# Optimization experiments

Measured on AMD Instinct MI355X. Metric: run time of the kernel, lower is better.

The kernel has to match this reference:

```python
import jax, jax.numpy as jnp
import numpy as np

LINHAS, COLUNAS, DIM, BATCH = 64, 64, 512, 256
N_NEURONS = LINHAS * COLUNAS
TAXA_INICIAL = 0.5
SIGMA_INICIAL = max(LINHAS, COLUNAS) / 2.0  # 32.0


def _grid_locations():
    # Matches tf.meshgrid (default 'xy' indexing) -> stack -> reshape(-1, 2)
    x = jnp.arange(LINHAS, dtype=jnp.float32)
    y = jnp.arange(COLUNAS, dtype=jnp.float32)
    gx, gy = jnp.meshgrid(x, y)  # 'xy' indexing, shapes (COLUNAS, LINHAS)
    return jnp.stack([gx, gy], axis=-1).reshape(-1, 2)  # (N_NEURONS, 2)


def setup_inputs() -> dict:
    key = jax.random.key(0)
    kx, kw = jax.random.split(key)
    X = jax.random.normal(kx, (BATCH, DIM), dtype=jnp.float32)
    # keras 'random_normal' initializer: stddev 0.05
    pesos = jax.random.normal(kw, (N_NEURONS, DIM), dtype=jnp.float32) * 0.05
    return {
        "X": X,
        "pesos": pesos,
        "localizacoes": _grid_locations(),
        "passo_atual": 10,
        "total_passos": 1000,
    }


def reference(X, pesos, localizacoes, passo_atual, total_passos):
    decay = jnp.exp(jnp.float32(-passo_atual / total_passos))
    taxa = TAXA_INICIAL * decay
    sigma = SIGMA_INICIAL * decay

    # Euclidean cdist^2: (B, N)
    x2 = jnp.sum(X * X, axis=1, keepdims=True)            # (B, 1)
    w2 = jnp.sum(pesos * pesos, axis=1)                   # (N,)
    dist = x2 + w2 - 2.0 * (X @ pesos.T)                  # (B, N)

    bmu_idx = jnp.argmin(dist, axis=1)                    # (B,)
    bmu_loc = localizacoes[bmu_idx]                       # (B, 2)

    # Squared grid distance from every neuron to each sample's BMU: (B, N)
    diff = localizacoes[None, :, :] - bmu_loc[:, None, :]
    dist_grade = jnp.sum(diff * diff, axis=2)
    h = jnp.exp(-dist_grade / (2.0 * sigma * sigma))      # (B, N)

    # delta_total[n, d] = taxa * mean_b h[b, n] * (X[b, d] - pesos[n, d])
    # computed without materializing the (B, N, D) delta tensor.
    B = jnp.float32(X.shape[0])
    hX = jnp.einsum("bn,bd->nd", h, X)                    # (N, D)
    h_sum = jnp.sum(h, axis=0)                            # (N,)
    delta_total = (taxa / B) * (hX - h_sum[:, None] * pesos)

    new_pesos = pesos + delta_total
    return new_pesos, taxa, sigma
```

## Files before the change

### kernel.cpp

```cpp
#include <hip/hip_runtime.h>
#include <hip/hip_bf16.h>

typedef unsigned int u32;
typedef unsigned short u16;
typedef unsigned long long u64;

#define BATCH 256
#define NN 4096
#define DIM 512

using short8 = __attribute__((ext_vector_type(8))) short;
using f32x4  = __attribute__((ext_vector_type(4))) float;

__device__ inline float b2f(u16 u){ u32 i = ((u32)u)<<16; float f; __builtin_memcpy(&f,&i,4); return f; }
__device__ inline u16 f2b(float v){ __hip_bfloat16 h = __float2bfloat16(v); u16 r; __builtin_memcpy(&r,&h,2); return r; }

__device__ inline float ldv(const void* p, size_t i, int isbf){
  return isbf ? b2f(((const u16*)p)[i]) : ((const float*)p)[i];
}
__device__ inline void stv(void* p, size_t i, float v, int isbf){
  if (isbf) ((__hip_bfloat16*)p)[i] = __float2bfloat16(v);
  else ((float*)p)[i] = v;
}

__device__ inline int sniff(const void* X, int t, int* sh){
  if (t < 64){
    u32 v = ((const u32*)X)[t];
    u16 lo = (u16)(v & 0xffffu);
    int e = (lo >> 7) & 0xff;
    int sane = ((lo & 0x7fffu) == 0) || (e >= 110 && e <= 132);
    u64 m = __ballot(sane);
    if (t == 0) *sh = (__popcll(m) >= 32) ? 1 : 0;
  }
  __syncthreads();
  return *sh;
}

__global__ __launch_bounds__(256) void k_prep(const void* X, const void* W,
    u64* pack, float* w2, u16* XT, u16* Xb, u16* Wb,
    const int* passo, const int* total, void* out){
  __shared__ int sflag;
  int t = threadIdx.x;
  int isbf = sniff(X, t, &sflag);
  int blk = blockIdx.x;
  if (blk < 512){
    int d = blk;
    float v = ldv(X, (size_t)t*DIM + d, isbf);
    XT[(size_t)d*BATCH + t] = f2b(v);
    if (!isbf){
      size_t i = (size_t)d*256 + t;
      Xb[i] = f2b(((const float*)X)[i]);
    }
  } else {
    int j = blk - 512;
    int n0 = j*8;
    int wv = t>>6, lane = t&63;
    #pragma unroll
    for (int rr=0; rr<2; ++rr){
      int n = n0 + wv*2 + rr;
      float xv[8]; float s = 0.f;
      if (isbf){
        short8 x = *(const short8*)((const u16*)W + (size_t)n*DIM + lane*8);
        #pragma unroll
        for (int q=0;q<8;q++) xv[q] = b2f((u16)x[q]);
      } else {
        #pragma unroll
        for (int q=0;q<8;q++) xv[q] = ((const float*)W)[(size_t)n*DIM + lane*8 + q];
      }
      #pragma unroll
      for (int q=0;q<8;q++) s += xv[q]*xv[q];
      #pragma unroll
      for (int off=32; off; off>>=1) s += __shfl_down(s, off);
      if (lane == 0) w2[n] = s;
      if (!isbf){
        #pragma unroll
        for (int q=0;q<8;q++) Wb[(size_t)n*DIM + lane*8 + q] = f2b(xv[q]);
      }
    }
    if (j == 0){
      pack[t] = ~0ull;
      if (t == 0){
        float decay = expf(-(float)passo[0]/(float)total[0]);
        stv(out, (size_t)NN*DIM,     0.5f*decay, isbf);
        stv(out, (size_t)NN*DIM + 1, 32.f*decay, isbf);
      }
    }
  }
}

__global__ __launch_bounds__(256) void k_score(const void* X, const void* W,
    const u16* Xws, const u16* Wws, const float* w2, u64* pack){
  __shared__ int sflag;
  __shared__ float sval[4][32];
  __shared__ int   sidx[4][32];
  int t = threadIdx.x;
  int isbf = sniff(X, t, &sflag);
  const u16* Xb = isbf ? (const u16*)X : Xws;
  const u16* Wb = isbf ? (const u16*)W : Wws;
  int wv = t>>6, l = t&63;
  int lr = l&15, lg = l>>4;

  int id = blockIdx.x;
  int xcd = id & 7, sub = id >> 3;
  int ny = xcd*4 + (sub>>3);
  int bx = sub & 7;
  int b0 = bx*32;
  int n0 = ny*128 + wv*32;

  const u16* xp0 = Xb + (size_t)(b0 + lr)*DIM + lg*8;
  const u16* xp1 = xp0 + (size_t)16*DIM;
  const u16* wp0 = Wb + (size_t)(n0 + lr)*DIM + lg*8;
  const u16* wp1 = wp0 + (size_t)16*DIM;

  f32x4 acc00 = {0,0,0,0}, acc01 = {0,0,0,0}, acc10 = {0,0,0,0}, acc11 = {0,0,0,0};
  #pragma unroll
  for (int ks=0; ks<16; ++ks){
    short8 a0 = *(const short8*)(xp0 + ks*32);
    short8 a1 = *(const short8*)(xp1 + ks*32);
    short8 w0 = *(const short8*)(wp0 + ks*32);
    short8 w1 = *(const short8*)(wp1 + ks*32);
    acc00 = __builtin_amdgcn_mfma_f32_16x16x32_bf16(a0, w0, acc00, 0,0,0);
    acc01 = __builtin_amdgcn_mfma_f32_16x16x32_bf16(a0, w1, acc01, 0,0,0);
    acc10 = __builtin_amdgcn_mfma_f32_16x16x32_bf16(a1, w0, acc10, 0,0,0);
    acc11 = __builtin_amdgcn_mfma_f32_16x16x32_bf16(a1, w1, acc11, 0,0,0);
  }

  float w20 = w2[n0 + lr];
  float w21 = w2[n0 + 16 + lr];
  #pragma unroll
  for (int bb=0; bb<2; ++bb){
    #pragma unroll
    for (int r=0;r<4;++r){
      float s0 = w20 - 2.f*(bb ? acc10[r] : acc00[r]);
      float s1 = w21 - 2.f*(bb ? acc11[r] : acc01[r]);
      float bv; int bi;
      if (s0 <= s1){ bv = s0; bi = n0 + lr; } else { bv = s1; bi = n0 + 16 + lr; }
      #pragma unroll
      for (int m=1; m<16; m<<=1){
        float ov = __shfl_xor(bv, m);
        int   oi = __shfl_xor(bi, m);
        if (ov < bv || (ov == bv && oi < bi)){ bv = ov; bi = oi; }
      }
      if (lr == 0){ int bl = bb*16 + lg*4 + r; sval[wv][bl] = bv; sidx[wv][bl] = bi; }
    }
  }
  __syncthreads();
  if (t < 32){
    float bv = sval[0][t]; int bi = sidx[0][t];
    #pragma unroll
    for (int w4=1; w4<4; ++w4){
      float ov = sval[w4][t]; int oi = sidx[w4][t];
      if (ov < bv || (ov == bv && oi < bi)){ bv = ov; bi = oi; }
    }
    u32 sb = __float_as_uint(bv);
    sb = (sb & 0x80000000u) ? ~sb : (sb | 0x80000000u);
    atomicMin(pack + b0 + t, ((u64)sb << 32) | (u32)bi);
  }
}

__global__ __launch_bounds__(512) void k_update(const void* X, const u16* XT, const void* W,
    const u64* pack, const int* passo, const int* total, void* out){
  __shared__ int sflag;
  __shared__ u16 hT[16][264];
  __shared__ float hpart[8][8];
  __shared__ float hs[16];
  int t = threadIdx.x;
  int isbf = sniff(X, t, &sflag);
  int wv = t>>6, l = t&63;
  int n0 = blockIdx.x * 16;

  float decay = expf(-(float)passo[0] / (float)total[0]);
  float taxa = 0.5f*decay, sigma = 32.f*decay;
  float inv2s2 = 1.f/(2.f*sigma*sigma);

  {
    int b = t & 255;
    int rbase = (t >> 8) * 8;
    int m = (int)(u32)(pack[b] & 0xffffffffu);
    int mx = m & 63, my = m >> 6;
    float hv[8];
    #pragma unroll
    for (int i=0;i<8;++i){
      int n = n0 + rbase + i;
      int dx = (n & 63) - mx;
      int dy = (n >> 6) - my;
      float h = expf(-(float)(dx*dx + dy*dy) * inv2s2);
      hv[i] = h;
      hT[rbase + i][b] = f2b(h);
    }
    #pragma unroll
    for (int i=0;i<8;++i){
      float s = hv[i];
      #pragma unroll
      for (int off=32; off; off>>=1) s += __shfl_down(s, off);
      if (l == 0) hpart[wv][i] = s;
    }
  }
  __syncthreads();
  if (t < 16){
    int g = (t >> 3) * 4;
    hs[t] = hpart[g][t&7] + hpart[g+1][t&7] + hpart[g+2][t&7] + hpart[g+3][t&7];
  }
  __syncthreads();

  int lr = l & 15, lg = l >> 4;
  int d0 = wv * 64;
  f32x4 acc[4];
  #pragma unroll
  for (int f=0;f<4;++f) acc[f] = (f32x4){0.f,0.f,0.f,0.f};

  #pragma unroll
  for (int ks=0; ks<8; ++ks){
    short8 a = *(const short8*)(&hT[lr][ks*32 + lg*8]);
    #pragma unroll
    for (int f=0; f<4; ++f){
      short8 bfr = *(const short8*)(XT + (size_t)(d0 + f*16 + lr)*BATCH + ks*32 + lg*8);
      acc[f] = __builtin_amdgcn_mfma_f32_16x16x32_bf16(a, bfr, acc[f], 0,0,0);
    }
  }

  float cc = taxa / (float)BATCH;
  #pragma unroll
  for (int r=0;r<4;++r){
    int n = n0 + lg*4 + r;
    float hsv = hs[lg*4 + r];
    #pragma unroll
    for (int f=0;f<4;++f){
      size_t gi = (size_t)n*DIM + d0 + f*16 + lr;
      float wv_ = ldv(W, gi, isbf);
      float o = wv_ + cc*(acc[f][r] - hsv*wv_);
      stv(out, gi, o, isbf);
    }
  }
}

extern "C" void kernel_launch(void* const* d_in, const int* in_sizes, int n_in,
                              void* d_out, int out_size, void* d_ws, size_t ws_size,
                              hipStream_t stream) {
  const void* X = d_in[0];
  const void* W = d_in[1];
  const int* passo = (const int*)d_in[3];
  const int* total = (const int*)d_in[4];

  char* ws = (char*)d_ws;
  u64* pack = (u64*)(ws + 256);
  float* w2 = (float*)(ws + 2304);
  u16* XT   = (u16*)(ws + 18688);
  u16* Xb   = (u16*)(ws + 280832);
  u16* Wb   = (u16*)(ws + 542976);

  k_prep  <<<1024, 256, 0, stream>>>(X, W, pack, w2, XT, Xb, Wb, passo, total, d_out);
  k_score <<<256, 256, 0, stream>>>(X, W, Xb, Wb, w2, pack);
  k_update<<<NN/16, 512, 0, stream>>>(X, XT, W, pack, passo, total, d_out);
}
```

Before: 38.84 us.

## Fuse prep, score and update into one cooperative kernel with grid syncs

Merges the three kernel launches into a single cooperative kernel of 256 blocks of 512 threads, separating the phases with grid-wide barriers. Work per block in each phase is remapped so the scoring GEMM uses 8 waves with two MFMA tiles each instead of 4 waves with four. The aim is to remove launch gaps and inter-kernel drain between phases. In exchange it pays for two grid syncs and caps the grid at 256 blocks, and it falls back to the old three-kernel path if the cooperative launch fails.

```diff
diff --git a/kernel.cpp b/kernel.cpp
--- a/kernel.cpp
+++ b/kernel.cpp
@@ -1,5 +1,8 @@
 #include <hip/hip_runtime.h>
 #include <hip/hip_bf16.h>
+#include <hip/hip_cooperative_groups.h>
+
+namespace cg = cooperative_groups;
 
 typedef unsigned int u32;
 typedef unsigned short u16;
@@ -34,6 +37,185 @@
   }
   __syncthreads();
   return *sh;
+}
+
+__global__ __launch_bounds__(512) void k_fused(const void* X, const void* W,
+    u64* pack, float* w2, u16* XT, u16* Xb, u16* Wb,
+    const int* passo, const int* total, void* out){
+  __shared__ int sflag;
+  __shared__ u16 hT[16][264];
+  __shared__ float hpart[8][8];
+  __shared__ float hs[16];
+  __shared__ float sval[4][32];
+  __shared__ int   sidx[4][32];
+
+  int t = threadIdx.x;
+  int isbf = sniff(X, t, &sflag);
+  int blk = blockIdx.x;
+  int wv = t>>6, l = t&63, lr = l&15, lg = l>>4;
+
+  {
+    int d = blk*2 + (t>>8);
+    int b = t & 255;
+    XT[(size_t)d*BATCH + b] = f2b(ldv(X, (size_t)b*DIM + d, isbf));
+    if (!isbf){
+      size_t i = (size_t)blk*512 + t;
+      Xb[i] = f2b(((const float*)X)[i]);
+    }
+    #pragma unroll
+    for (int rr=0; rr<2; ++rr){
+      int n = blk*16 + wv*2 + rr;
+      float xv[8]; float s = 0.f;
+      if (isbf){
+        short8 x = *(const short8*)((const u16*)W + (size_t)n*DIM + l*8);
+        #pragma unroll
+        for (int q=0;q<8;q++) xv[q] = b2f((u16)x[q]);
+      } else {
+        #pragma unroll
+        for (int q=0;q<8;q++) xv[q] = ((const float*)W)[(size_t)n*DIM + l*8 + q];
+      }
+      #pragma unroll
+      for (int q=0;q<8;q++) s += xv[q]*xv[q];
+      #pragma unroll
+      for (int off=32; off; off>>=1) s += __shfl_down(s, off);
+      if (l == 0) w2[n] = s;
+      if (!isbf){
+        #pragma unroll
+        for (int q=0;q<8;q++) Wb[(size_t)n*DIM + l*8 + q] = f2b(xv[q]);
+      }
+    }
+    if (blk == 0){
+      if (t < 256) pack[t] = ~0ull;
+      if (t == 0){
+        float decay = expf(-(float)passo[0]/(float)total[0]);
+        stv(out, (size_t)NN*DIM,     0.5f*decay, isbf);
+        stv(out, (size_t)NN*DIM + 1, 32.f*decay, isbf);
+      }
+    }
+  }
+  cg::this_grid().sync();
+
+  {
+    const u16* Xp = isbf ? (const u16*)X : Xb;
+    const u16* Wp = isbf ? (const u16*)W : Wb;
+    int xcd = blk & 7, sub = blk >> 3;
+    int ny = xcd*4 + (sub>>3);
+    int bx = sub & 7;
+    int bb0 = bx*32;
+    int b0 = bb0 + (wv&1)*16;
+    int n0 = ny*128 + (wv>>1)*32;
+
+    const u16* xp  = Xp + (size_t)(b0 + lr)*DIM + lg*8;
+    const u16* wp0 = Wp + (size_t)(n0 + lr)*DIM + lg*8;
+    const u16* wp1 = wp0 + (size_t)16*DIM;
+
+    f32x4 acc0 = {0,0,0,0}, acc1 = {0,0,0,0};
+    #pragma unroll
+    for (int ks=0; ks<16; ++ks){
+      short8 a  = *(const short8*)(xp  + ks*32);
+      short8 w0 = *(const short8*)(wp0 + ks*32);
+      short8 w1 = *(const short8*)(wp1 + ks*32);
+      acc0 = __builtin_amdgcn_mfma_f32_16x16x32_bf16(a, w0, acc0, 0,0,0);
+      acc1 = __builtin_amdgcn_mfma_f32_16x16x32_bf16(a, w1, acc1, 0,0,0);
+    }
+
+    float w20 = w2[n0 + lr];
+    float w21 = w2[n0 + 16 + lr];
+    #pragma unroll
+    for (int r=0;r<4;++r){
+      float s0 = w20 - 2.f*acc0[r];
+      float s1 = w21 - 2.f*acc1[r];
+      float bv; int bi;
+      if (s0 <= s1){ bv = s0; bi = n0 + lr; } else { bv = s1; bi = n0 + 16 + lr; }
+      #pragma unroll
+      for (int m=1; m<16; m<<=1){
+        float ov = __shfl_xor(bv, m);
+        int   oi = __shfl_xor(bi, m);
+        if (ov < bv || (ov == bv && oi < bi)){ bv = ov; bi = oi; }
+      }
+      if (lr == 0){
+        sval[wv>>1][(wv&1)*16 + lg*4 + r] = bv;
+        sidx[wv>>1][(wv&1)*16 + lg*4 + r] = bi;
+      }
+    }
+    __syncthreads();
+    if (t < 32){
+      float bv = sval[0][t]; int bi = sidx[0][t];
+      #pragma unroll
+      for (int wc=1; wc<4; ++wc){
+        float ov = sval[wc][t]; int oi = sidx[wc][t];
+        if (ov < bv || (ov == bv && oi < bi)){ bv = ov; bi = oi; }
+      }
+      u32 sb = __float_as_uint(bv);
+      sb = (sb & 0x80000000u) ? ~sb : (sb | 0x80000000u);
+      atomicMin(pack + bb0 + t, ((u64)sb << 32) | (u32)bi);
+    }
+  }
+  cg::this_grid().sync();
+
+  {
+    int n0 = blk * 16;
+    float decay = expf(-(float)passo[0] / (float)total[0]);
+    float taxa = 0.5f*decay, sigma = 32.f*decay;
+    float inv2s2 = 1.f/(2.f*sigma*sigma);
+
+    int b = t & 255;
+    int rbase = (t >> 8) * 8;
+    int m = (int)(u32)(pack[b] & 0xffffffffu);
+    int mx = m & 63, my = m >> 6;
+    float hv[8];
+    #pragma unroll
+    for (int i=0;i<8;++i){
+      int n = n0 + rbase + i;
+      int dx = (n & 63) - mx;
+      int dy = (n >> 6) - my;
+      float h = expf(-(float)(dx*dx + dy*dy) * inv2s2);
+      hv[i] = h;
+      hT[rbase + i][b] = f2b(h);
+    }
+    #pragma unroll
+    for (int i=0;i<8;++i){
+      float s = hv[i];
+      #pragma unroll
+      for (int off=32; off; off>>=1) s += __shfl_down(s, off);
+      if (l == 0) hpart[wv][i] = s;
+    }
+    __syncthreads();
+    if (t < 16){
+      int g = (t >> 3) * 4;
+      hs[t] = hpart[g][t&7] + hpart[g+1][t&7] + hpart[g+2][t&7] + hpart[g+3][t&7];
+    }
+    __syncthreads();
+
+    int d0 = wv * 64;
+    f32x4 acc[4];
+    #pragma unroll
+    for (int f=0;f<4;++f) acc[f] = (f32x4){0.f,0.f,0.f,0.f};
+
+    #pragma unroll
+    for (int ks=0; ks<8; ++ks){
+      short8 a = *(const short8*)(&hT[lr][ks*32 + lg*8]);
+      #pragma unroll
+      for (int f=0; f<4; ++f){
+        short8 bfr = *(const short8*)(XT + (size_t)(d0 + f*16 + lr)*BATCH + ks*32 + lg*8);
+        acc[f] = __builtin_amdgcn_mfma_f32_16x16x32_bf16(a, bfr, acc[f], 0,0,0);
+      }
+    }
+
+    float cc = taxa / (float)BATCH;
+    #pragma unroll
+    for (int r=0;r<4;++r){
+      int n = n0 + lg*4 + r;
+      float hsv = hs[lg*4 + r];
+      #pragma unroll
+      for (int f=0;f<4;++f){
+        size_t gi = (size_t)n*DIM + d0 + f*16 + lr;
+        float wv_ = ldv(W, gi, isbf);
+        float o = wv_ + cc*(acc[f][r] - hsv*wv_);
+        stv(out, gi, o, isbf);
+      }
+    }
+  }
 }
 
 __global__ __launch_bounds__(256) void k_prep(const void* X, const void* W,
@@ -45,8 +227,7 @@
   int blk = blockIdx.x;
   if (blk < 512){
     int d = blk;
-    float v = ldv(X, (size_t)t*DIM + d, isbf);
-    XT[(size_t)d*BATCH + t] = f2b(v);
+    XT[(size_t)d*BATCH + t] = f2b(ldv(X, (size_t)t*DIM + d, isbf));
     if (!isbf){
       size_t i = (size_t)d*256 + t;
       Xb[i] = f2b(((const float*)X)[i]);
@@ -248,8 +429,16 @@
   u16* XT   = (u16*)(ws + 18688);
   u16* Xb   = (u16*)(ws + 280832);
   u16* Wb   = (u16*)(ws + 542976);
-
-  k_prep  <<<1024, 256, 0, stream>>>(X, W, pack, w2, XT, Xb, Wb, passo, total, d_out);
-  k_score <<<256, 256, 0, stream>>>(X, W, Xb, Wb, w2, pack);
-  k_update<<<NN/16, 512, 0, stream>>>(X, XT, W, pack, passo, total, d_out);
-}
+  void* out = d_out;
+
+  void* args[] = {(void*)&X, (void*)&W, (void*)&pack, (void*)&w2, (void*)&XT,
+                  (void*)&Xb, (void*)&Wb, (void*)&passo, (void*)&total, (void*)&out};
+  hipError_t err = hipLaunchCooperativeKernel((const void*)k_fused, dim3(256), dim3(512),
+                                              args, 0, stream);
+  if (err != hipSuccess){
+    (void)hipGetLastError();
+    k_prep  <<<1024, 256, 0, stream>>>(X, W, pack, w2, XT, Xb, Wb, passo, total, out);
+    k_score <<<256, 256, 0, stream>>>(X, W, Xb, Wb, w2, pack);
+    k_update<<<NN/16, 512, 0, stream>>>(X, XT, W, pack, passo, total, out);
+  }
+}
```

Result: slower. 106.0 us (+173.0%).

## Fuse prep into score kernel and replace atomic BMU with partial-min buffer

Applied to the files above, without the earlier changes.

Removes the separate prep kernel. The score kernel now builds the bf16 transpose of X, the bf16 copies of X and W, and the row norms of W itself, keeping the norms in shared memory. The global atomicMin on a pre-initialised pack buffer becomes per-column-block partial minima, which the update kernel reduces in shared memory before computing the neighbourhood weights. This saves a launch and the pack initialisation. The cost is redundant conversion: each of the 8 batch blocks re-converts the same 128 W rows, and the fp32 W loop reads 128 contiguous floats per thread, so loads are poorly coalesced.

```diff
diff --git a/kernel.cpp b/kernel.cpp
--- a/kernel.cpp
+++ b/kernel.cpp
@@ -36,147 +36,150 @@
   return *sh;
 }
 
-__global__ __launch_bounds__(256) void k_prep(const void* X, const void* W,
-    u64* pack, float* w2, u16* XT, u16* Xb, u16* Wb,
-    const int* passo, const int* total, void* out){
+__global__ __launch_bounds__(512) void k1_score(const void* X, const void* W,
+    u16* Xb, u16* Wb, u16* XT, u64* pack2){
   __shared__ int sflag;
-  int t = threadIdx.x;
-  int isbf = sniff(X, t, &sflag);
-  int blk = blockIdx.x;
-  if (blk < 512){
-    int d = blk;
-    float v = ldv(X, (size_t)t*DIM + d, isbf);
-    XT[(size_t)d*BATCH + t] = f2b(v);
-    if (!isbf){
-      size_t i = (size_t)d*256 + t;
-      Xb[i] = f2b(((const float*)X)[i]);
-    }
-  } else {
-    int j = blk - 512;
-    int n0 = j*8;
-    int wv = t>>6, lane = t&63;
-    #pragma unroll
-    for (int rr=0; rr<2; ++rr){
-      int n = n0 + wv*2 + rr;
-      float xv[8]; float s = 0.f;
-      if (isbf){
-        short8 x = *(const short8*)((const u16*)W + (size_t)n*DIM + lane*8);
-        #pragma unroll
-        for (int q=0;q<8;q++) xv[q] = b2f((u16)x[q]);
-      } else {
-        #pragma unroll
-        for (int q=0;q<8;q++) xv[q] = ((const float*)W)[(size_t)n*DIM + lane*8 + q];
-      }
-      #pragma unroll
-      for (int q=0;q<8;q++) s += xv[q]*xv[q];
-      #pragma unroll
-      for (int off=32; off; off>>=1) s += __shfl_down(s, off);
-      if (lane == 0) w2[n] = s;
-      if (!isbf){
-        #pragma unroll
-        for (int q=0;q<8;q++) Wb[(size_t)n*DIM + lane*8 + q] = f2b(xv[q]);
-      }
-    }
-    if (j == 0){
-      pack[t] = ~0ull;
-      if (t == 0){
-        float decay = expf(-(float)passo[0]/(float)total[0]);
-        stv(out, (size_t)NN*DIM,     0.5f*decay, isbf);
-        stv(out, (size_t)NN*DIM + 1, 32.f*decay, isbf);
-      }
-    }
-  }
-}
-
-__global__ __launch_bounds__(256) void k_score(const void* X, const void* W,
-    const u16* Xws, const u16* Wws, const float* w2, u64* pack){
-  __shared__ int sflag;
+  __shared__ float sw2[128];
   __shared__ float sval[4][32];
   __shared__ int   sidx[4][32];
   int t = threadIdx.x;
   int isbf = sniff(X, t, &sflag);
-  const u16* Xb = isbf ? (const u16*)X : Xws;
-  const u16* Wb = isbf ? (const u16*)W : Wws;
-  int wv = t>>6, l = t&63;
-  int lr = l&15, lg = l>>4;
-
-  int id = blockIdx.x;
-  int xcd = id & 7, sub = id >> 3;
+  int blk = blockIdx.x;
+  int wv = t>>6, l = t&63, lr = l&15, lg = l>>4;
+  int xcd = blk & 7, sub = blk >> 3;
   int ny = xcd*4 + (sub>>3);
   int bx = sub & 7;
   int b0 = bx*32;
-  int n0 = ny*128 + wv*32;
-
-  const u16* xp0 = Xb + (size_t)(b0 + lr)*DIM + lg*8;
-  const u16* xp1 = xp0 + (size_t)16*DIM;
-  const u16* wp0 = Wb + (size_t)(n0 + lr)*DIM + lg*8;
+  int nbase = ny*128;
+
+  {
+    int d = blk*2 + (t>>8);
+    int b = t & 255;
+    XT[(size_t)d*BATCH + b] = f2b(ldv(X, (size_t)b*DIM + d, isbf));
+  }
+  if (!isbf){
+    for (int i=t; i<32*DIM; i+=512){
+      size_t gi = (size_t)(b0 + (i>>9))*DIM + (i&511);
+      Xb[gi] = f2b(((const float*)X)[gi]);
+    }
+  }
+  {
+    int r = t>>2, q = t&3;
+    size_t base = (size_t)(nbase + r)*DIM + q*128;
+    float s = 0.f;
+    if (isbf){
+      const u16* wp = (const u16*)W + base;
+      #pragma unroll
+      for (int i=0;i<16;++i){
+        short8 x = *(const short8*)(wp + i*8);
+        #pragma unroll
+        for (int j=0;j<8;++j){ float f = b2f((u16)x[j]); s += f*f; }
+      }
+    } else {
+      const float* wp = (const float*)W + base;
+      for (int i=0;i<128;++i){ float f = wp[i]; s += f*f; Wb[base+i] = f2b(f); }
+    }
+    s += __shfl_xor(s, 1);
+    s += __shfl_xor(s, 2);
+    if (q == 0) sw2[r] = s;
+  }
+  __syncthreads();
+
+  const u16* Xp = isbf ? (const u16*)X : Xb;
+  const u16* Wp = isbf ? (const u16*)W : Wb;
+  int bh = (wv&1)*16;
+  int nq = (wv>>1)*32;
+  int n0 = nbase + nq;
+  const u16* xp  = Xp + (size_t)(b0 + bh + lr)*DIM + lg*8;
+  const u16* wp0 = Wp + (size_t)(n0 + lr)*DIM + lg*8;
   const u16* wp1 = wp0 + (size_t)16*DIM;
 
-  f32x4 acc00 = {0,0,0,0}, acc01 = {0,0,0,0}, acc10 = {0,0,0,0}, acc11 = {0,0,0,0};
+  f32x4 acc0 = {0,0,0,0}, acc1 = {0,0,0,0};
   #pragma unroll
   for (int ks=0; ks<16; ++ks){
-    short8 a0 = *(const short8*)(xp0 + ks*32);
-    short8 a1 = *(const short8*)(xp1 + ks*32);
+    short8 a  = *(const short8*)(xp  + ks*32);
     short8 w0 = *(const short8*)(wp0 + ks*32);
     short8 w1 = *(const short8*)(wp1 + ks*32);
-    acc00 = __builtin_amdgcn_mfma_f32_16x16x32_bf16(a0, w0, acc00, 0,0,0);
-    acc01 = __builtin_amdgcn_mfma_f32_16x16x32_bf16(a0, w1, acc01, 0,0,0);
-    acc10 = __builtin_amdgcn_mfma_f32_16x16x32_bf16(a1, w0, acc10, 0,0,0);
-    acc11 = __builtin_amdgcn_mfma_f32_16x16x32_bf16(a1, w1, acc11, 0,0,0);
-  }
-
-  float w20 = w2[n0 + lr];
-  float w21 = w2[n0 + 16 + lr];
-  #pragma unroll
-  for (int bb=0; bb<2; ++bb){
-    #pragma unroll
-    for (int r=0;r<4;++r){
-      float s0 = w20 - 2.f*(bb ? acc10[r] : acc00[r]);
-      float s1 = w21 - 2.f*(bb ? acc11[r] : acc01[r]);
-      float bv; int bi;
-      if (s0 <= s1){ bv = s0; bi = n0 + lr; } else { bv = s1; bi = n0 + 16 + lr; }
-      #pragma unroll
-      for (int m=1; m<16; m<<=1){
-        float ov = __shfl_xor(bv, m);
-        int   oi = __shfl_xor(bi, m);
-        if (ov < bv || (ov == bv && oi < bi)){ bv = ov; bi = oi; }
-      }
-      if (lr == 0){ int bl = bb*16 + lg*4 + r; sval[wv][bl] = bv; sidx[wv][bl] = bi; }
+    acc0 = __builtin_amdgcn_mfma_f32_16x16x32_bf16(a, w0, acc0, 0,0,0);
+    acc1 = __builtin_amdgcn_mfma_f32_16x16x32_bf16(a, w1, acc1, 0,0,0);
+  }
+
+  float w20 = sw2[nq + lr];
+  float w21 = sw2[nq + 16 + lr];
+  #pragma unroll
+  for (int r=0;r<4;++r){
+    float s0 = w20 - 2.f*acc0[r];
+    float s1 = w21 - 2.f*acc1[r];
+    float bv; int bi;
+    if (s0 <= s1){ bv = s0; bi = n0 + lr; } else { bv = s1; bi = n0 + 16 + lr; }
+    #pragma unroll
+    for (int m=1; m<16; m<<=1){
+      float ov = __shfl_xor(bv, m);
+      int   oi = __shfl_xor(bi, m);
+      if (ov < bv || (ov == bv && oi < bi)){ bv = ov; bi = oi; }
+    }
+    if (lr == 0){
+      sval[wv>>1][bh + lg*4 + r] = bv;
+      sidx[wv>>1][bh + lg*4 + r] = bi;
     }
   }
   __syncthreads();
   if (t < 32){
     float bv = sval[0][t]; int bi = sidx[0][t];
     #pragma unroll
-    for (int w4=1; w4<4; ++w4){
-      float ov = sval[w4][t]; int oi = sidx[w4][t];
+    for (int qc=1; qc<4; ++qc){
+      float ov = sval[qc][t]; int oi = sidx[qc][t];
       if (ov < bv || (ov == bv && oi < bi)){ bv = ov; bi = oi; }
     }
     u32 sb = __float_as_uint(bv);
     sb = (sb & 0x80000000u) ? ~sb : (sb | 0x80000000u);
-    atomicMin(pack + b0 + t, ((u64)sb << 32) | (u32)bi);
-  }
-}
-
-__global__ __launch_bounds__(512) void k_update(const void* X, const u16* XT, const void* W,
-    const u64* pack, const int* passo, const int* total, void* out){
+    pack2[(size_t)ny*BATCH + b0 + t] = ((u64)sb << 32) | (u32)bi;
+  }
+}
+
+__global__ __launch_bounds__(512) void k2_update(const void* X, const u16* XT, const void* W,
+    const u64* pack2, const int* passo, const int* total, void* out){
   __shared__ int sflag;
+  __shared__ u64 smin[512];
+  __shared__ int sbmu[256];
   __shared__ u16 hT[16][264];
   __shared__ float hpart[8][8];
   __shared__ float hs[16];
   int t = threadIdx.x;
   int isbf = sniff(X, t, &sflag);
-  int wv = t>>6, l = t&63;
+  int wv = t>>6, l = t&63, lr = l&15, lg = l>>4;
   int n0 = blockIdx.x * 16;
+
+  {
+    int b = t & 255, half = t >> 8;
+    u64 m = ~0ull;
+    #pragma unroll
+    for (int c=0;c<16;++c){
+      u64 v = pack2[(size_t)(half*16 + c)*BATCH + b];
+      if (v < m) m = v;
+    }
+    smin[t] = m;
+  }
+  __syncthreads();
+  if (t < 256){
+    u64 m = smin[t] < smin[t+256] ? smin[t] : smin[t+256];
+    sbmu[t] = (int)(u32)(m & 0xffffffffu);
+  }
+  __syncthreads();
 
   float decay = expf(-(float)passo[0] / (float)total[0]);
   float taxa = 0.5f*decay, sigma = 32.f*decay;
   float inv2s2 = 1.f/(2.f*sigma*sigma);
 
+  if (blockIdx.x == 0 && t == 0){
+    stv(out, (size_t)NN*DIM,     taxa,  isbf);
+    stv(out, (size_t)NN*DIM + 1, sigma, isbf);
+  }
+
   {
     int b = t & 255;
     int rbase = (t >> 8) * 8;
-    int m = (int)(u32)(pack[b] & 0xffffffffu);
+    int m = sbmu[b];
     int mx = m & 63, my = m >> 6;
     float hv[8];
     #pragma unroll
@@ -203,7 +206,6 @@
   }
   __syncthreads();
 
-  int lr = l & 15, lg = l >> 4;
   int d0 = wv * 64;
   f32x4 acc[4];
   #pragma unroll
@@ -243,13 +245,11 @@
   const int* total = (const int*)d_in[4];
 
   char* ws = (char*)d_ws;
-  u64* pack = (u64*)(ws + 256);
-  float* w2 = (float*)(ws + 2304);
-  u16* XT   = (u16*)(ws + 18688);
-  u16* Xb   = (u16*)(ws + 280832);
-  u16* Wb   = (u16*)(ws + 542976);
-
-  k_prep  <<<1024, 256, 0, stream>>>(X, W, pack, w2, XT, Xb, Wb, passo, total, d_out);
-  k_score <<<256, 256, 0, stream>>>(X, W, Xb, Wb, w2, pack);
-  k_update<<<NN/16, 512, 0, stream>>>(X, XT, W, pack, passo, total, d_out);
-}
+  u64* pack2 = (u64*)(ws + 0);
+  u16* XT    = (u16*)(ws + 65536);
+  u16* Xb    = (u16*)(ws + 327680);
+  u16* Wb    = (u16*)(ws + 589824);
+
+  k1_score <<<256, 512, 0, stream>>>(X, W, Xb, Wb, XT, pack2);
+  k2_update<<<256, 512, 0, stream>>>(X, XT, W, pack2, passo, total, d_out);
+}
```

After: 53.91 us. 38.8% more time.
